# Optimization experiments

Measured on AMD Instinct MI355X. Metric: run time of the kernel, lower is better.

Reference implementation:

```python
import jax, jax.numpy as jnp
import numpy as np

EPS = 1e-5
C = 1.0
SQRT_C = 1.0
MAX_NORM = 0.95


def _log0(y):
    # log map at origin: atanh(sqrt(c)||y||) * y / (sqrt(c)||y||)
    norm = jnp.clip(jnp.linalg.norm(y, axis=-1, keepdims=True), EPS)
    arg = jnp.clip(SQRT_C * norm, None, 1.0 - EPS)
    return jnp.arctanh(arg) * y / (SQRT_C * norm)


def _exp0(v):
    # exp map at origin: tanh(sqrt(c)||v||) * v / (sqrt(c)||v||)
    norm = jnp.clip(jnp.linalg.norm(v, axis=-1, keepdims=True), EPS)
    return jnp.tanh(SQRT_C * norm) * v / (SQRT_C * norm)


def _proj(x):
    # project onto Poincare ball of radius MAX_NORM/sqrt(c)
    max_r = MAX_NORM / SQRT_C
    norm = jnp.linalg.norm(x, axis=-1, keepdims=True)
    return jnp.where(norm > max_r, x * max_r / jnp.clip(norm, EPS), x)


def _hyp_linear(x, W, b):
    # log -> euclidean linear -> exp -> project
    v = _log0(x)
    v = v @ W.T + b
    return _proj(_exp0(v))


def _hyp_graph_conv(x, src, dst, n_nodes, Wm, bm, Wu, bu):
    # 1. hyperbolic linear message transform
    h = _hyp_linear(x, Wm, bm)
    # 2. tangent-space (hyperbolic) mean aggregation over incoming edges
    t = _log0(h[src])                                   # [E, D]
    summed = jax.ops.segment_sum(t, dst, num_segments=n_nodes)
    cnt = jax.ops.segment_sum(jnp.ones((src.shape[0], 1), t.dtype), dst,
                              num_segments=n_nodes)
    agg = _proj(_exp0(summed / jnp.clip(cnt, 1.0)))
    # 3. hyperbolic linear update
    return _hyp_linear(agg, Wu, bu)


def setup_inputs() -> dict:
    key = jax.random.key(0)
    k1, k2, k3, k4 = jax.random.split(key, 4)
    N, E, D, L = 50000, 800000, 128, 2
    x = jax.random.normal(k1, (N, D), dtype=jnp.float32) * 0.01
    edge_index = jax.random.randint(k2, (2, E), 0, N, dtype=jnp.int32)
    msg_W = jax.random.normal(k3, (L, D, D), dtype=jnp.float32) * 0.05
    msg_b = jnp.zeros((L, D), dtype=jnp.float32)
    upd_W = jax.random.normal(k4, (L, D, D), dtype=jnp.float32) * 0.05
    upd_b = jnp.zeros((L, D), dtype=jnp.float32)
    return {"x": x, "edge_index": edge_index, "msg_W": msg_W, "msg_b": msg_b,
            "upd_W": upd_W, "upd_b": upd_b}


def reference(x, edge_index, msg_W, msg_b, upd_W, upd_b):
    src, dst = edge_index[0], edge_index[1]
    n_nodes = x.shape[0]
    h = x
    for l in range(msg_W.shape[0]):  # small fixed layer count
        h = _hyp_graph_conv(h, src, dst, n_nodes,
                            msg_W[l], msg_b[l], upd_W[l], upd_b[l])
    return h
```

## Files before the change

### kernel.cpp

```cpp
#include <hip/hip_runtime.h>
#include <math.h>

#define EPSF 1e-5f
#define MAXN 0.95f
#define DD 128

typedef unsigned short u16;
typedef __attribute__((ext_vector_type(8))) __bf16 bf16x8;
typedef __attribute__((ext_vector_type(4))) float f32x4;
typedef __attribute__((ext_vector_type(8))) unsigned short u16x8;
typedef __attribute__((ext_vector_type(4))) unsigned u32x4;

__device__ __forceinline__ u16 f2bf(float f) {
    unsigned u = __float_as_uint(f);
    return (u16)((u + 0x7FFFu + ((u >> 16) & 1u)) >> 16);
}
__device__ __forceinline__ float bf2f(u16 b) {
    return __uint_as_float(((unsigned)b) << 16);
}

__device__ __forceinline__ float chain_scale(float nrm, bool log_out) {
    float nc  = fmaxf(nrm, EPSF);
    float f   = tanhf(nc) / nc;
    float wn  = f * nrm;
    float p   = (wn > MAXN) ? (MAXN / fmaxf(wn, EPSF)) : 1.f;
    float s   = f * p;
    if (log_out) {
        float n2  = wn * p;
        float n2c = fmaxf(n2, EPSF);
        float arg = fminf(n2c, 1.f - EPSF);
        s *= atanhf(arg) / n2c;
    }
    return s;
}

__global__ __launch_bounds__(256)
void split_w(const float* __restrict__ msgW, const float* __restrict__ updW,
             u16* __restrict__ whi, u16* __restrict__ wlo, int L)
{
    int gid = blockIdx.x * 256 + threadIdx.x;
    int total = L * 2 * DD * DD;
    if (gid >= total) return;
    int mat = gid >> 14;
    int elem = gid & (DD * DD - 1);
    int l = mat >> 1, tpe = mat & 1;
    float f = (tpe ? updW : msgW)[(size_t)l * DD * DD + elem];
    u16 hb = f2bf(f);
    whi[gid] = hb;
    wlo[gid] = f2bf(f - bf2f(hb));
}

template<int LOG_OUT, int LO_OUT, int FP32_OUT, int F32_IN, int SCALE_IN>
__global__ __launch_bounds__(256)
void mfma_linear(const u16* __restrict__ vhi, const u16* __restrict__ vlo,
                 const float* __restrict__ xin, const float* __restrict__ sIn,
                 const u16* __restrict__ whi, const u16* __restrict__ wlo,
                 const float* __restrict__ bias,
                 u16* __restrict__ ohi, u16* __restrict__ olo,
                 float* __restrict__ ofp, int N)
{
    __shared__ float sred[4][64];
    __shared__ float sScale[64];
    __shared__ float sSin[SCALE_IN ? 64 : 1];
    __shared__ u16 sHi[FP32_OUT ? 1 : 64][144];
    __shared__ u16 sLo[LO_OUT ? 64 : 1][144];

    const int tid  = threadIdx.x;
    const int w    = tid >> 6;
    const int lane = tid & 63;
    const int l15  = lane & 15, lk = lane >> 4;
    const int base = blockIdx.x * 64;

    if (SCALE_IN) {
        if (tid < 64) {
            int rg = base + tid;
            sSin[tid] = sIn[rg < N ? rg : (N - 1)];
        }
        __syncthreads();
    }

    bf16x8 wh[2][4], wl[2][4];
    #pragma unroll
    for (int nt = 0; nt < 2; ++nt) {
        const int j = w * 32 + nt * 16 + l15;
        #pragma unroll
        for (int kt = 0; kt < 4; ++kt) {
            const int off = j * DD + kt * 32 + lk * 8;
            wh[nt][kt] = *(const bf16x8*)(whi + off);
            wl[nt][kt] = *(const bf16x8*)(wlo + off);
        }
    }
    const float bv0 = bias[w * 32 + l15];
    const float bv1 = bias[w * 32 + 16 + l15];

    f32x4 acc[4][2];
    #pragma unroll
    for (int mt = 0; mt < 4; ++mt)
        #pragma unroll
        for (int nt = 0; nt < 2; ++nt)
            acc[mt][nt] = (f32x4){0.f, 0.f, 0.f, 0.f};

    #pragma unroll
    for (int mt = 0; mt < 4; ++mt) {
        int row = base + mt * 16 + l15;
        row = (row < N) ? row : (N - 1);
        bf16x8 ah[4], al[4];
        if (F32_IN) {
            const float* xr = xin + (size_t)row * DD + lk * 8;
            float fv[32];
            float ss = 0.f;
            #pragma unroll
            for (int kt = 0; kt < 4; ++kt) {
                float4 a = *(const float4*)(xr + kt * 32);
                float4 b = *(const float4*)(xr + kt * 32 + 4);
                fv[kt*8+0]=a.x; fv[kt*8+1]=a.y; fv[kt*8+2]=a.z; fv[kt*8+3]=a.w;
                fv[kt*8+4]=b.x; fv[kt*8+5]=b.y; fv[kt*8+6]=b.z; fv[kt*8+7]=b.w;
            }
            #pragma unroll
            for (int q = 0; q < 32; ++q) ss += fv[q] * fv[q];
            ss += __shfl_xor(ss, 16);
            ss += __shfl_xor(ss, 32);
            float nc = fmaxf(sqrtf(ss), EPSF);
            float sc = atanhf(fminf(nc, 1.f - EPSF)) / nc;
            #pragma unroll
            for (int kt = 0; kt < 4; ++kt) {
                u16x8 uh, ul;
                #pragma unroll
                for (int q = 0; q < 8; ++q) {
                    float t = fv[kt*8+q] * sc;
                    u16 hb = f2bf(t);
                    uh[q] = hb;
                    ul[q] = f2bf(t - bf2f(hb));
                }
                ah[kt] = *reinterpret_cast<bf16x8*>(&uh);
                al[kt] = *reinterpret_cast<bf16x8*>(&ul);
            }
        } else {
            const size_t ro = (size_t)row * DD + lk * 8;
            #pragma unroll
            for (int kt = 0; kt < 4; ++kt) {
                ah[kt] = *(const bf16x8*)(vhi + ro + kt * 32);
                al[kt] = *(const bf16x8*)(vlo + ro + kt * 32);
            }
        }
        #pragma unroll
        for (int kt = 0; kt < 4; ++kt) {
            #pragma unroll
            for (int nt = 0; nt < 2; ++nt) {
                acc[mt][nt] = __builtin_amdgcn_mfma_f32_16x16x32_bf16(
                    ah[kt], wh[nt][kt], acc[mt][nt], 0, 0, 0);
                acc[mt][nt] = __builtin_amdgcn_mfma_f32_16x16x32_bf16(
                    al[kt], wh[nt][kt], acc[mt][nt], 0, 0, 0);
                acc[mt][nt] = __builtin_amdgcn_mfma_f32_16x16x32_bf16(
                    ah[kt], wl[nt][kt], acc[mt][nt], 0, 0, 0);
            }
        }
    }

    #pragma unroll
    for (int mt = 0; mt < 4; ++mt) {
        #pragma unroll
        for (int r = 0; r < 4; ++r) {
            const float sv = SCALE_IN ? sSin[mt*16 + lk*4 + r] : 1.f;
            float y0 = acc[mt][0][r] * sv + bv0;
            float y1 = acc[mt][1][r] * sv + bv1;
            float part = y0 * y0 + y1 * y1;
            part += __shfl_xor(part, 1);
            part += __shfl_xor(part, 2);
            part += __shfl_xor(part, 4);
            part += __shfl_xor(part, 8);
            if (l15 == 0) sred[w][mt*16 + lk*4 + r] = part;
        }
    }
    __syncthreads();
    if (tid < 64) {
        float ss = sred[0][tid] + sred[1][tid] + sred[2][tid] + sred[3][tid];
        sScale[tid] = chain_scale(sqrtf(ss), LOG_OUT != 0);
    }
    __syncthreads();

    #pragma unroll
    for (int mt = 0; mt < 4; ++mt) {
        #pragma unroll
        for (int r = 0; r < 4; ++r) {
            const int rloc = mt*16 + lk*4 + r;
            const float s = sScale[rloc];
            const float sv = SCALE_IN ? sSin[rloc] : 1.f;
            #pragma unroll
            for (int nt = 0; nt < 2; ++nt) {
                float z = (acc[mt][nt][r] * sv + (nt ? bv1 : bv0)) * s;
                const int col = w*32 + nt*16 + l15;
                if (FP32_OUT) {
                    const int rg = base + rloc;
                    if (rg < N) ofp[(size_t)rg * DD + col] = z;
                } else {
                    u16 hb = f2bf(z);
                    sHi[rloc][col] = hb;
                    if (LO_OUT) sLo[rloc][col] = f2bf(z - bf2f(hb));
                }
            }
        }
    }
    if (!FP32_OUT) {
        __syncthreads();
        const int row = tid >> 2, qc = (tid & 3) * 32;
        const int rg = base + row;
        if (rg < N) {
            #pragma unroll
            for (int i = 0; i < 4; ++i)
                *(u16x8*)(ohi + (size_t)rg * DD + qc + i*8) =
                    *(const u16x8*)(&sHi[row][qc + i*8]);
            if (LO_OUT) {
                #pragma unroll
                for (int i = 0; i < 4; ++i)
                    *(u16x8*)(olo + (size_t)rg * DD + qc + i*8) =
                        *(const u16x8*)(&sLo[row][qc + i*8]);
            }
        }
    }
}

__global__ __launch_bounds__(256)
void degree_rank(const int* __restrict__ dst, int* __restrict__ deg,
                 int* __restrict__ rank, int E)
{
    int e4 = (blockIdx.x * 256 + threadIdx.x) * 4;
    if (e4 + 3 < E) {
        int4 d = *(const int4*)(dst + e4);
        int4 r;
        r.x = atomicAdd(&deg[d.x], 1);
        r.y = atomicAdd(&deg[d.y], 1);
        r.z = atomicAdd(&deg[d.z], 1);
        r.w = atomicAdd(&deg[d.w], 1);
        *(int4*)(rank + e4) = r;
    } else {
        for (int e = e4; e < E; ++e) rank[e] = atomicAdd(&deg[dst[e]], 1);
    }
}

__global__ __launch_bounds__(1024)
void scan_rowptr(const int* __restrict__ deg, int* __restrict__ rowptr, int N)
{
    __shared__ int wsum[16];
    const int t = threadIdx.x, wv = t >> 6, ln = t & 63;
    int carry = 0;
    const int nch = (N + 4095) / 4096;
    for (int c = 0; c < nch; ++c) {
        const int i = c * 4096 + t * 4;
        int4 d = *(const int4*)(deg + i);
        int e1 = d.x, e2 = e1 + d.y, e3 = e2 + d.z, tot = e3 + d.w;
        int sc = tot;
        #pragma unroll
        for (int off = 1; off < 64; off <<= 1) {
            int u = __shfl_up(sc, off);
            if (ln >= off) sc += u;
        }
        if (ln == 63) wsum[wv] = sc;
        __syncthreads();
        if (wv == 0 && ln < 16) {
            int s2 = wsum[ln];
            #pragma unroll
            for (int off = 1; off < 16; off <<= 1) {
                int u = __shfl_up(s2, off);
                if (ln >= off) s2 += u;
            }
            wsum[ln] = s2;
        }
        __syncthreads();
        const int off0 = carry + ((wv > 0) ? wsum[wv - 1] : 0) + (sc - tot);
        if (i + 3 < N) {
            *(int4*)(rowptr + i) = make_int4(off0, off0 + e1, off0 + e2, off0 + e3);
        } else {
            if (i     < N) rowptr[i]     = off0;
            if (i + 1 < N) rowptr[i + 1] = off0 + e1;
            if (i + 2 < N) rowptr[i + 2] = off0 + e2;
        }
        carry += wsum[15];
        __syncthreads();
    }
    if (t == 0) rowptr[N] = carry;
}

__global__ __launch_bounds__(256)
void fill_csr(const int* __restrict__ src, const int* __restrict__ dst,
              const int* __restrict__ rowptr, const int* __restrict__ rank,
              int* __restrict__ csr, int E)
{
    int e4 = (blockIdx.x * 256 + threadIdx.x) * 4;
    if (e4 + 3 < E) {
        int4 d = *(const int4*)(dst + e4);
        int4 r = *(const int4*)(rank + e4);
        int4 s = *(const int4*)(src + e4);
        csr[rowptr[d.x] + r.x] = s.x;
        csr[rowptr[d.y] + r.y] = s.y;
        csr[rowptr[d.z] + r.z] = s.z;
        csr[rowptr[d.w] + r.w] = s.w;
    } else {
        for (int e = e4; e < E; ++e) csr[rowptr[dst[e]] + rank[e]] = src[e];
    }
}

__global__ __launch_bounds__(256)
void csr_gather_sum(const u16* __restrict__ ghi, const int* __restrict__ rowptr,
                    const int* __restrict__ csr, u16* __restrict__ ohi,
                    u16* __restrict__ olo, float* __restrict__ ssum, int N)
{
    int node = blockIdx.x * 4 + (threadIdx.x >> 6);
    if (node >= N) return;
    const int lane = threadIdx.x & 63;
    const int eg = lane >> 4, l15 = lane & 15;
    const int beg = rowptr[node], end = rowptr[node + 1];

    float acc[8] = {0.f,0.f,0.f,0.f,0.f,0.f,0.f,0.f};
    for (int b = beg; b < end; b += 64) {
        const int cnt = min(end - b, 64);
        const int myidx = (lane < cnt) ? csr[b + lane] : 0;
        u32x4 vc;
        {
            const bool act = eg < cnt;
            const int s = __shfl(myidx, act ? eg : 0);
            if (act) vc = *(const u32x4*)(ghi + (size_t)s * DD + l15 * 8);
        }
        for (int j = 0; j < cnt; j += 4) {
            const int en = j + 4 + eg;
            const bool actn = en < cnt;
            const int sn = __shfl(myidx, actn ? en : 0);
            u32x4 vn;
            if (actn) vn = *(const u32x4*)(ghi + (size_t)sn * DD + l15 * 8);
            if (j + eg < cnt) {
                #pragma unroll
                for (int p = 0; p < 4; ++p) {
                    acc[2*p+0] += __uint_as_float(vc[p] << 16);
                    acc[2*p+1] += __uint_as_float(vc[p] & 0xffff0000u);
                }
            }
            vc = vn;
        }
    }
    #pragma unroll
    for (int q = 0; q < 8; ++q) {
        acc[q] += __shfl_xor(acc[q], 16);
        acc[q] += __shfl_xor(acc[q], 32);
    }
    float ss = 0.f;
    #pragma unroll
    for (int q = 0; q < 8; ++q) ss += acc[q] * acc[q];
    ss += __shfl_xor(ss, 1); ss += __shfl_xor(ss, 2);
    ss += __shfl_xor(ss, 4); ss += __shfl_xor(ss, 8);
    if (eg == 0) {
        u32x4 hw, lw;
        #pragma unroll
        for (int p = 0; p < 4; ++p) {
            u16 h0 = f2bf(acc[2*p+0]), h1 = f2bf(acc[2*p+1]);
            hw[p] = (unsigned)h0 | ((unsigned)h1 << 16);
            u16 l0 = f2bf(acc[2*p+0] - bf2f(h0));
            u16 l1 = f2bf(acc[2*p+1] - bf2f(h1));
            lw[p] = (unsigned)l0 | ((unsigned)l1 << 16);
        }
        *(u32x4*)(ohi + (size_t)node * DD + l15 * 8) = hw;
        *(u32x4*)(olo + (size_t)node * DD + l15 * 8) = lw;
        if (l15 == 0) ssum[node] = ss;
    }
}

__global__ __launch_bounds__(256)
void node_scale(const float* __restrict__ ssum, const int* __restrict__ rowptr,
                float* __restrict__ sout, int N)
{
    int n = blockIdx.x * 256 + threadIdx.x;
    if (n >= N) return;
    int cnt = max(rowptr[n + 1] - rowptr[n], 1);
    float inv = 1.f / (float)cnt;
    float nrm = sqrtf(ssum[n]) * inv;
    sout[n] = chain_scale(nrm, true) * inv;
}

extern "C" void kernel_launch(void* const* d_in, const int* in_sizes, int n_in,
                              void* d_out, int out_size, void* d_ws, size_t ws_size,
                              hipStream_t stream)
{
    const float* x     = (const float*)d_in[0];
    const int*   ei    = (const int*)d_in[1];
    const float* msg_W = (const float*)d_in[2];
    const float* msg_b = (const float*)d_in[3];
    const float* upd_W = (const float*)d_in[4];
    const float* upd_b = (const float*)d_in[5];

    const int N = in_sizes[0] / DD;
    const int E = in_sizes[1] / 2;
    const int L = in_sizes[2] / (DD * DD);

    const int* src = ei;
    const int* dst = ei + E;

    u16* Ahi  = (u16*)d_ws;
    u16* Alo  = Ahi + (size_t)N * DD;
    u16* WhiA = Alo + (size_t)N * DD;
    u16* WloA = WhiA + (size_t)2 * L * DD * DD;
    int* deg  = (int*)(WloA + (size_t)2 * L * DD * DD);
    const int degCap = ((N + 4095) / 4096) * 4096;
    int* rowptr = deg + degCap;
    int* csr    = rowptr + (N + 1);
    float* ssum   = (float*)(csr + E);
    float* sscale = ssum + N;

    u16* Bhi = (u16*)d_out;
    u16* Blo = Bhi + (size_t)N * DD;
    int* rank = (int*)Blo;

    u16* bufHi[2] = {Ahi, Bhi};
    u16* bufLo[2] = {Alo, Blo};
    int cur = (L % 2 == 0) ? 1 : 0;

    const int nodeBlocks = (N + 63) / 64;
    const int aggBlocks  = (N + 3) / 4;
    const int edge4Blocks = ((E + 3) / 4 + 255) / 256;

    hipMemsetAsync(deg, 0, (size_t)degCap * sizeof(int), stream);
    degree_rank<<<edge4Blocks, 256, 0, stream>>>(dst, deg, rank, E);
    scan_rowptr<<<1, 1024, 0, stream>>>(deg, rowptr, N);
    fill_csr<<<edge4Blocks, 256, 0, stream>>>(src, dst, rowptr, rank, csr, E);
    split_w<<<(2 * L * DD * DD + 255) / 256, 256, 0, stream>>>(
        msg_W, upd_W, WhiA, WloA, L);

    for (int l = 0; l < L; ++l) {
        const u16* wmh = WhiA + (size_t)(l * 2 + 0) * DD * DD;
        const u16* wml = WloA + (size_t)(l * 2 + 0) * DD * DD;
        const u16* wuh = WhiA + (size_t)(l * 2 + 1) * DD * DD;
        const u16* wul = WloA + (size_t)(l * 2 + 1) * DD * DD;

        if (l == 0)
            mfma_linear<1, 0, 0, 1, 0><<<nodeBlocks, 256, 0, stream>>>(
                nullptr, nullptr, x, nullptr, wmh, wml, msg_b + (size_t)l * DD,
                bufHi[cur ^ 1], nullptr, nullptr, N);
        else
            mfma_linear<1, 0, 0, 0, 0><<<nodeBlocks, 256, 0, stream>>>(
                bufHi[cur], bufLo[cur], nullptr, nullptr, wmh, wml,
                msg_b + (size_t)l * DD, bufHi[cur ^ 1], nullptr, nullptr, N);
        cur ^= 1;

        csr_gather_sum<<<aggBlocks, 256, 0, stream>>>(
            bufHi[cur], rowptr, csr, bufHi[cur ^ 1], bufLo[cur ^ 1], ssum, N);
        cur ^= 1;

        node_scale<<<(N + 255) / 256, 256, 0, stream>>>(ssum, rowptr, sscale, N);

        if (l == L - 1)
            mfma_linear<0, 0, 1, 0, 1><<<nodeBlocks, 256, 0, stream>>>(
                bufHi[cur], bufLo[cur], nullptr, sscale, wuh, wul,
                upd_b + (size_t)l * DD, nullptr, nullptr, (float*)d_out, N);
        else
            mfma_linear<1, 1, 0, 0, 1><<<nodeBlocks, 256, 0, stream>>>(
                bufHi[cur], bufLo[cur], nullptr, sscale, wuh, wul,
                upd_b + (size_t)l * DD, bufHi[cur ^ 1], bufLo[cur ^ 1], nullptr, N);
        cur ^= 1;
    }
}
```

Baseline: 277.5 us.

## Fuse update and next message linear, inline node scale, drop lo outputs

Merges the update linear of layer l with the message linear of layer l+1 into one kernel. The intermediate hi/lo bf16 activations stay in LDS instead of making a global round trip. The separate node_scale kernel is removed and its per-row scale is computed inline from ssum and rowptr. The memset is replaced by a small zeroing kernel, and the LDS row padding changes. This cuts launches and global traffic, but the fused kernel uses more LDS and registers, which may lower occupancy.

```diff
diff --git a/kernel.cpp b/kernel.cpp
--- a/kernel.cpp
+++ b/kernel.cpp
@@ -34,6 +34,21 @@
     return s;
 }
 
+__device__ __forceinline__ float agg_scale(const float* __restrict__ ssum,
+                                           const int* __restrict__ rowptr,
+                                           int rg) {
+    int cnt = max(rowptr[rg + 1] - rowptr[rg], 1);
+    float inv = 1.f / (float)cnt;
+    return chain_scale(sqrtf(ssum[rg]) * inv, true) * inv;
+}
+
+__global__ __launch_bounds__(256)
+void zero_int4(int4* __restrict__ p, int n4)
+{
+    int i = blockIdx.x * 256 + threadIdx.x;
+    if (i < n4) p[i] = make_int4(0, 0, 0, 0);
+}
+
 __global__ __launch_bounds__(256)
 void split_w(const float* __restrict__ msgW, const float* __restrict__ updW,
              u16* __restrict__ whi, u16* __restrict__ wlo, int L)
@@ -50,20 +65,19 @@
     wlo[gid] = f2bf(f - bf2f(hb));
 }
 
-template<int LOG_OUT, int LO_OUT, int FP32_OUT, int F32_IN, int SCALE_IN>
+template<int LOG_OUT, int FP32_OUT, int F32_IN, int SCALE_IN>
 __global__ __launch_bounds__(256)
 void mfma_linear(const u16* __restrict__ vhi, const u16* __restrict__ vlo,
-                 const float* __restrict__ xin, const float* __restrict__ sIn,
+                 const float* __restrict__ xin,
+                 const float* __restrict__ ssum, const int* __restrict__ rowptr,
                  const u16* __restrict__ whi, const u16* __restrict__ wlo,
                  const float* __restrict__ bias,
-                 u16* __restrict__ ohi, u16* __restrict__ olo,
-                 float* __restrict__ ofp, int N)
+                 u16* __restrict__ ohi, float* __restrict__ ofp, int N)
 {
     __shared__ float sred[4][64];
     __shared__ float sScale[64];
     __shared__ float sSin[SCALE_IN ? 64 : 1];
-    __shared__ u16 sHi[FP32_OUT ? 1 : 64][144];
-    __shared__ u16 sLo[LO_OUT ? 64 : 1][144];
+    __shared__ u16 sHi[FP32_OUT ? 1 : 64][136];
 
     const int tid  = threadIdx.x;
     const int w    = tid >> 6;
@@ -74,7 +88,7 @@
     if (SCALE_IN) {
         if (tid < 64) {
             int rg = base + tid;
-            sSin[tid] = sIn[rg < N ? rg : (N - 1)];
+            sSin[tid] = agg_scale(ssum, rowptr, rg < N ? rg : (N - 1));
         }
         __syncthreads();
     }
@@ -194,9 +208,7 @@
                     const int rg = base + rloc;
                     if (rg < N) ofp[(size_t)rg * DD + col] = z;
                 } else {
-                    u16 hb = f2bf(z);
-                    sHi[rloc][col] = hb;
-                    if (LO_OUT) sLo[rloc][col] = f2bf(z - bf2f(hb));
+                    sHi[rloc][col] = f2bf(z);
                 }
             }
         }
@@ -210,12 +222,211 @@
             for (int i = 0; i < 4; ++i)
                 *(u16x8*)(ohi + (size_t)rg * DD + qc + i*8) =
                     *(const u16x8*)(&sHi[row][qc + i*8]);
-            if (LO_OUT) {
+        }
+    }
+}
+
+__global__ __launch_bounds__(256)
+void mfma_linear_fused(const u16* __restrict__ vhi, const u16* __restrict__ vlo,
+                       const float* __restrict__ ssum, const int* __restrict__ rowptr,
+                       const u16* __restrict__ wuh, const u16* __restrict__ wul,
+                       const float* __restrict__ bu,
+                       const u16* __restrict__ wmh, const u16* __restrict__ wml,
+                       const float* __restrict__ bm,
+                       u16* __restrict__ ohi, int N)
+{
+    __shared__ float sred[4][64];
+    __shared__ float sScale[64];
+    __shared__ float sSin[64];
+    __shared__ u16 sHi[64][136];
+    __shared__ u16 sLo[64][136];
+
+    const int tid  = threadIdx.x;
+    const int w    = tid >> 6;
+    const int lane = tid & 63;
+    const int l15  = lane & 15, lk = lane >> 4;
+    const int base = blockIdx.x * 64;
+
+    if (tid < 64) {
+        int rg = base + tid;
+        sSin[tid] = agg_scale(ssum, rowptr, rg < N ? rg : (N - 1));
+    }
+    __syncthreads();
+
+    f32x4 acc[4][2];
+
+    {
+        bf16x8 wh[2][4], wl[2][4];
+        #pragma unroll
+        for (int nt = 0; nt < 2; ++nt) {
+            const int j = w * 32 + nt * 16 + l15;
+            #pragma unroll
+            for (int kt = 0; kt < 4; ++kt) {
+                const int off = j * DD + kt * 32 + lk * 8;
+                wh[nt][kt] = *(const bf16x8*)(wuh + off);
+                wl[nt][kt] = *(const bf16x8*)(wul + off);
+            }
+        }
+        const float bv0 = bu[w * 32 + l15];
+        const float bv1 = bu[w * 32 + 16 + l15];
+
+        #pragma unroll
+        for (int mt = 0; mt < 4; ++mt)
+            #pragma unroll
+            for (int nt = 0; nt < 2; ++nt)
+                acc[mt][nt] = (f32x4){0.f, 0.f, 0.f, 0.f};
+
+        #pragma unroll
+        for (int mt = 0; mt < 4; ++mt) {
+            int row = base + mt * 16 + l15;
+            row = (row < N) ? row : (N - 1);
+            const size_t ro = (size_t)row * DD + lk * 8;
+            bf16x8 ah[4], al[4];
+            #pragma unroll
+            for (int kt = 0; kt < 4; ++kt) {
+                ah[kt] = *(const bf16x8*)(vhi + ro + kt * 32);
+                al[kt] = *(const bf16x8*)(vlo + ro + kt * 32);
+            }
+            #pragma unroll
+            for (int kt = 0; kt < 4; ++kt) {
                 #pragma unroll
-                for (int i = 0; i < 4; ++i)
-                    *(u16x8*)(olo + (size_t)rg * DD + qc + i*8) =
-                        *(const u16x8*)(&sLo[row][qc + i*8]);
-            }
+                for (int nt = 0; nt < 2; ++nt) {
+                    acc[mt][nt] = __builtin_amdgcn_mfma_f32_16x16x32_bf16(
+                        ah[kt], wh[nt][kt], acc[mt][nt], 0, 0, 0);
+                    acc[mt][nt] = __builtin_amdgcn_mfma_f32_16x16x32_bf16(
+                        al[kt], wh[nt][kt], acc[mt][nt], 0, 0, 0);
+                    acc[mt][nt] = __builtin_amdgcn_mfma_f32_16x16x32_bf16(
+                        ah[kt], wl[nt][kt], acc[mt][nt], 0, 0, 0);
+                }
+            }
+        }
+
+        #pragma unroll
+        for (int mt = 0; mt < 4; ++mt) {
+            #pragma unroll
+            for (int r = 0; r < 4; ++r) {
+                const float sv = sSin[mt*16 + lk*4 + r];
+                float y0 = acc[mt][0][r] * sv + bv0;
+                float y1 = acc[mt][1][r] * sv + bv1;
+                float part = y0 * y0 + y1 * y1;
+                part += __shfl_xor(part, 1);
+                part += __shfl_xor(part, 2);
+                part += __shfl_xor(part, 4);
+                part += __shfl_xor(part, 8);
+                if (l15 == 0) sred[w][mt*16 + lk*4 + r] = part;
+            }
+        }
+        __syncthreads();
+        if (tid < 64) {
+            float ss = sred[0][tid] + sred[1][tid] + sred[2][tid] + sred[3][tid];
+            sScale[tid] = chain_scale(sqrtf(ss), true);
+        }
+        __syncthreads();
+        #pragma unroll
+        for (int mt = 0; mt < 4; ++mt) {
+            #pragma unroll
+            for (int r = 0; r < 4; ++r) {
+                const int rloc = mt*16 + lk*4 + r;
+                const float s = sScale[rloc];
+                const float sv = sSin[rloc];
+                #pragma unroll
+                for (int nt = 0; nt < 2; ++nt) {
+                    float z = (acc[mt][nt][r] * sv + (nt ? bv1 : bv0)) * s;
+                    const int col = w*32 + nt*16 + l15;
+                    u16 hb = f2bf(z);
+                    sHi[rloc][col] = hb;
+                    sLo[rloc][col] = f2bf(z - bf2f(hb));
+                }
+            }
+        }
+    }
+    __syncthreads();
+
+    {
+        bf16x8 wh[2][4], wl[2][4];
+        #pragma unroll
+        for (int nt = 0; nt < 2; ++nt) {
+            const int j = w * 32 + nt * 16 + l15;
+            #pragma unroll
+            for (int kt = 0; kt < 4; ++kt) {
+                const int off = j * DD + kt * 32 + lk * 8;
+                wh[nt][kt] = *(const bf16x8*)(wmh + off);
+                wl[nt][kt] = *(const bf16x8*)(wml + off);
+            }
+        }
+        const float bv0 = bm[w * 32 + l15];
+        const float bv1 = bm[w * 32 + 16 + l15];
+
+        #pragma unroll
+        for (int mt = 0; mt < 4; ++mt)
+            #pragma unroll
+            for (int nt = 0; nt < 2; ++nt)
+                acc[mt][nt] = (f32x4){0.f, 0.f, 0.f, 0.f};
+
+        #pragma unroll
+        for (int mt = 0; mt < 4; ++mt) {
+            const int r16 = mt * 16 + l15;
+            bf16x8 ah[4], al[4];
+            #pragma unroll
+            for (int kt = 0; kt < 4; ++kt) {
+                ah[kt] = *(const bf16x8*)(&sHi[r16][kt * 32 + lk * 8]);
+                al[kt] = *(const bf16x8*)(&sLo[r16][kt * 32 + lk * 8]);
+            }
+            #pragma unroll
+            for (int kt = 0; kt < 4; ++kt) {
+                #pragma unroll
+                for (int nt = 0; nt < 2; ++nt) {
+                    acc[mt][nt] = __builtin_amdgcn_mfma_f32_16x16x32_bf16(
+                        ah[kt], wh[nt][kt], acc[mt][nt], 0, 0, 0);
+                    acc[mt][nt] = __builtin_amdgcn_mfma_f32_16x16x32_bf16(
+                        al[kt], wh[nt][kt], acc[mt][nt], 0, 0, 0);
+                    acc[mt][nt] = __builtin_amdgcn_mfma_f32_16x16x32_bf16(
+                        ah[kt], wl[nt][kt], acc[mt][nt], 0, 0, 0);
+                }
+            }
+        }
+
+        #pragma unroll
+        for (int mt = 0; mt < 4; ++mt) {
+            #pragma unroll
+            for (int r = 0; r < 4; ++r) {
+                float y0 = acc[mt][0][r] + bv0;
+                float y1 = acc[mt][1][r] + bv1;
+                float part = y0 * y0 + y1 * y1;
+                part += __shfl_xor(part, 1);
+                part += __shfl_xor(part, 2);
+                part += __shfl_xor(part, 4);
+                part += __shfl_xor(part, 8);
+                if (l15 == 0) sred[w][mt*16 + lk*4 + r] = part;
+            }
+        }
+        __syncthreads();
+        if (tid < 64) {
+            float ss = sred[0][tid] + sred[1][tid] + sred[2][tid] + sred[3][tid];
+            sScale[tid] = chain_scale(sqrtf(ss), true);
+        }
+        __syncthreads();
+        #pragma unroll
+        for (int mt = 0; mt < 4; ++mt) {
+            #pragma unroll
+            for (int r = 0; r < 4; ++r) {
+                const int rloc = mt*16 + lk*4 + r;
+                const float s = sScale[rloc];
+                #pragma unroll
+                for (int nt = 0; nt < 2; ++nt) {
+                    float z = (acc[mt][nt][r] + (nt ? bv1 : bv0)) * s;
+                    sHi[rloc][w*32 + nt*16 + l15] = f2bf(z);
+                }
+            }
+        }
+        __syncthreads();
+        const int row = tid >> 2, qc = (tid & 3) * 32;
+        const int rg = base + row;
+        if (rg < N) {
+            #pragma unroll
+            for (int i = 0; i < 4; ++i)
+                *(u16x8*)(ohi + (size_t)rg * DD + qc + i*8) =
+                    *(const u16x8*)(&sHi[row][qc + i*8]);
         }
     }
 }
@@ -363,18 +574,6 @@
     }
 }
 
-__global__ __launch_bounds__(256)
-void node_scale(const float* __restrict__ ssum, const int* __restrict__ rowptr,
-                float* __restrict__ sout, int N)
-{
-    int n = blockIdx.x * 256 + threadIdx.x;
-    if (n >= N) return;
-    int cnt = max(rowptr[n + 1] - rowptr[n], 1);
-    float inv = 1.f / (float)cnt;
-    float nrm = sqrtf(ssum[n]) * inv;
-    sout[n] = chain_scale(nrm, true) * inv;
-}
-
 extern "C" void kernel_launch(void* const* d_in, const int* in_sizes, int n_in,
                               void* d_out, int out_size, void* d_ws, size_t ws_size,
                               hipStream_t stream)
@@ -401,58 +600,47 @@
     const int degCap = ((N + 4095) / 4096) * 4096;
     int* rowptr = deg + degCap;
     int* csr    = rowptr + (N + 1);
-    float* ssum   = (float*)(csr + E);
-    float* sscale = ssum + N;
-
-    u16* Bhi = (u16*)d_out;
-    u16* Blo = Bhi + (size_t)N * DD;
+    float* ssum = (float*)(csr + E);
+
+    u16* Bhi  = (u16*)d_out;
+    u16* Blo  = Bhi + (size_t)N * DD;
     int* rank = (int*)Blo;
 
-    u16* bufHi[2] = {Ahi, Bhi};
-    u16* bufLo[2] = {Alo, Blo};
-    int cur = (L % 2 == 0) ? 1 : 0;
-
-    const int nodeBlocks = (N + 63) / 64;
-    const int aggBlocks  = (N + 3) / 4;
+    const int nodeBlocks  = (N + 63) / 64;
+    const int aggBlocks   = (N + 3) / 4;
     const int edge4Blocks = ((E + 3) / 4 + 255) / 256;
 
-    hipMemsetAsync(deg, 0, (size_t)degCap * sizeof(int), stream);
+    zero_int4<<<(degCap / 4 + 255) / 256, 256, 0, stream>>>((int4*)deg, degCap / 4);
     degree_rank<<<edge4Blocks, 256, 0, stream>>>(dst, deg, rank, E);
     scan_rowptr<<<1, 1024, 0, stream>>>(deg, rowptr, N);
     fill_csr<<<edge4Blocks, 256, 0, stream>>>(src, dst, rowptr, rank, csr, E);
     split_w<<<(2 * L * DD * DD + 255) / 256, 256, 0, stream>>>(
         msg_W, upd_W, WhiA, WloA, L);
 
+    mfma_linear<1, 0, 1, 0><<<nodeBlocks, 256, 0, stream>>>(
+        nullptr, nullptr, x, nullptr, nullptr,
+        WhiA, WloA, msg_b, Bhi, nullptr, N);
+
     for (int l = 0; l < L; ++l) {
-        const u16* wmh = WhiA + (size_t)(l * 2 + 0) * DD * DD;
-        const u16* wml = WloA + (size_t)(l * 2 + 0) * DD * DD;
         const u16* wuh = WhiA + (size_t)(l * 2 + 1) * DD * DD;
         const u16* wul = WloA + (size_t)(l * 2 + 1) * DD * DD;
 
-        if (l == 0)
-            mfma_linear<1, 0, 0, 1, 0><<<nodeBlocks, 256, 0, stream>>>(
-                nullptr, nullptr, x, nullptr, wmh, wml, msg_b + (size_t)l * DD,
-                bufHi[cur ^ 1], nullptr, nullptr, N);
-        else
-            mfma_linear<1, 0, 0, 0, 0><<<nodeBlocks, 256, 0, stream>>>(
-                bufHi[cur], bufLo[cur], nullptr, nullptr, wmh, wml,
-                msg_b + (size_t)l * DD, bufHi[cur ^ 1], nullptr, nullptr, N);
-        cur ^= 1;
-
         csr_gather_sum<<<aggBlocks, 256, 0, stream>>>(
-            bufHi[cur], rowptr, csr, bufHi[cur ^ 1], bufLo[cur ^ 1], ssum, N);
-        cur ^= 1;
-
-        node_scale<<<(N + 255) / 256, 256, 0, stream>>>(ssum, rowptr, sscale, N);
-
-        if (l == L - 1)
-            mfma_linear<0, 0, 1, 0, 1><<<nodeBlocks, 256, 0, stream>>>(
-                bufHi[cur], bufLo[cur], nullptr, sscale, wuh, wul,
-                upd_b + (size_t)l * DD, nullptr, nullptr, (float*)d_out, N);
-        else
-            mfma_linear<1, 1, 0, 0, 1><<<nodeBlocks, 256, 0, stream>>>(
-                bufHi[cur], bufLo[cur], nullptr, sscale, wuh, wul,
-                upd_b + (size_t)l * DD, bufHi[cur ^ 1], bufLo[cur ^ 1], nullptr, N);
-        cur ^= 1;
-    }
-}
+            Bhi, rowptr, csr, Ahi, Alo, ssum, N);
+
+        if (l < L - 1) {
+            const u16* wmh = WhiA + (size_t)((l + 1) * 2 + 0) * DD * DD;
+            const u16* wml = WloA + (size_t)((l + 1) * 2 + 0) * DD * DD;
+            mfma_linear_fused<<<nodeBlocks, 256, 0, stream>>>(
+                Ahi, Alo, ssum, rowptr,
+                wuh, wul, upd_b + (size_t)l * DD,
+                wmh, wml, msg_b + (size_t)(l + 1) * DD,
+                Bhi, N);
+        } else {
+            mfma_linear<0, 1, 0, 1><<<nodeBlocks, 256, 0, stream>>>(
+                Ahi, Alo, nullptr, ssum, rowptr,
+                wuh, wul, upd_b + (size_t)l * DD,
+                nullptr, (float*)d_out, N);
+        }
+    }
+}
```

After: 255.1 us. -8.1%, faster.

## Fuse update and next message linear, fold node scale into GEMM, per-wave row tiles

Applied to the files above, without the earlier changes.

The MFMA linear kernel is restructured so each wave owns 16 rows and all 128 output columns. The row-norm reduction becomes an in-wave shuffle instead of cross-wave shared-memory reductions with block barriers. The node_scale kernel is removed: the per-node aggregation scale is computed inline from ssum and rowptr. The update linear of layer l and the message linear of layer l+1 are fused into one kernel that passes the intermediate through swizzled LDS, which also drops the lo-part global write. Weights are now streamed from global or cache per MFMA rather than held in registers, and the memset is replaced by a small zeroing kernel.

```diff
diff --git a/kernel.cpp b/kernel.cpp
--- a/kernel.cpp
+++ b/kernel.cpp
@@ -10,6 +10,8 @@
 typedef __attribute__((ext_vector_type(4))) float f32x4;
 typedef __attribute__((ext_vector_type(8))) unsigned short u16x8;
 typedef __attribute__((ext_vector_type(4))) unsigned u32x4;
+
+#define MFMA16 __builtin_amdgcn_mfma_f32_16x16x32_bf16
 
 __device__ __forceinline__ u16 f2bf(float f) {
     unsigned u = __float_as_uint(f);
@@ -34,6 +36,284 @@
     return s;
 }
 
+__device__ __forceinline__ float agg_scale(const float* __restrict__ ssum,
+                                           const int* __restrict__ rowptr,
+                                           int rg) {
+    int cnt = max(rowptr[rg + 1] - rowptr[rg], 1);
+    float inv = 1.f / (float)cnt;
+    return chain_scale(sqrtf(ssum[rg]) * inv, true) * inv;
+}
+
+__device__ __forceinline__ void gemm16(const bf16x8 ah[4], const bf16x8 al[4],
+                                       const u16* __restrict__ whi,
+                                       const u16* __restrict__ wlo,
+                                       int l15, int lk, f32x4 acc[8])
+{
+    #pragma unroll
+    for (int kt = 0; kt < 4; ++kt) {
+        #pragma unroll
+        for (int nt = 0; nt < 8; ++nt) {
+            const int off = (nt * 16 + l15) * DD + kt * 32 + lk * 8;
+            const bf16x8 wwh = *(const bf16x8*)(whi + off);
+            const bf16x8 wwl = *(const bf16x8*)(wlo + off);
+            acc[nt] = MFMA16(ah[kt], wwh, acc[nt], 0, 0, 0);
+            acc[nt] = MFMA16(al[kt], wwh, acc[nt], 0, 0, 0);
+            acc[nt] = MFMA16(ah[kt], wwl, acc[nt], 0, 0, 0);
+        }
+    }
+}
+
+__device__ __forceinline__ void loadA_bf(const u16* __restrict__ vhi,
+                                         const u16* __restrict__ vlo,
+                                         size_t ro, bf16x8 ah[4], bf16x8 al[4])
+{
+    #pragma unroll
+    for (int kt = 0; kt < 4; ++kt) {
+        ah[kt] = *(const bf16x8*)(vhi + ro + kt * 32);
+        al[kt] = *(const bf16x8*)(vlo + ro + kt * 32);
+    }
+}
+
+__device__ __forceinline__ void loadA_f32log(const float* __restrict__ xr,
+                                             bf16x8 ah[4], bf16x8 al[4])
+{
+    float fv[32]; float ss = 0.f;
+    #pragma unroll
+    for (int kt = 0; kt < 4; ++kt) {
+        float4 a = *(const float4*)(xr + kt * 32);
+        float4 b = *(const float4*)(xr + kt * 32 + 4);
+        fv[kt*8+0]=a.x; fv[kt*8+1]=a.y; fv[kt*8+2]=a.z; fv[kt*8+3]=a.w;
+        fv[kt*8+4]=b.x; fv[kt*8+5]=b.y; fv[kt*8+6]=b.z; fv[kt*8+7]=b.w;
+    }
+    #pragma unroll
+    for (int q = 0; q < 32; ++q) ss += fv[q] * fv[q];
+    ss += __shfl_xor(ss, 16);
+    ss += __shfl_xor(ss, 32);
+    float nc = fmaxf(sqrtf(ss), EPSF);
+    float sc = atanhf(fminf(nc, 1.f - EPSF)) / nc;
+    #pragma unroll
+    for (int kt = 0; kt < 4; ++kt) {
+        u16x8 uh, ul;
+        #pragma unroll
+        for (int q = 0; q < 8; ++q) {
+            float t = fv[kt*8+q] * sc;
+            u16 hb = f2bf(t);
+            uh[q] = hb;
+            ul[q] = f2bf(t - bf2f(hb));
+        }
+        ah[kt] = *reinterpret_cast<bf16x8*>(&uh);
+        al[kt] = *reinterpret_cast<bf16x8*>(&ul);
+    }
+}
+
+__device__ __forceinline__ void store_g_staged(u16* __restrict__ sg,
+                                               const f32x4 acc[8],
+                                               const float bv[8],
+                                               const float svr[4],
+                                               const float sr[4],
+                                               int l15, int lk, int lane,
+                                               int rowbase, u16* __restrict__ ohi,
+                                               int N)
+{
+    #pragma unroll
+    for (int r = 0; r < 4; ++r) {
+        const int row = lk * 4 + r;
+        const int key = (row & 7) << 3;
+        #pragma unroll
+        for (int nt = 0; nt < 8; ++nt) {
+            const int col = nt * 16 + l15;
+            float z = fmaf(acc[nt][r], svr[r], bv[nt]) * sr[r];
+            sg[row * 128 + ((col & ~7) ^ key) + (col & 7)] = f2bf(z);
+        }
+    }
+    asm volatile("s_waitcnt lgkmcnt(0)" ::: "memory");
+    __builtin_amdgcn_sched_barrier(0);
+    {
+        const int row = lane >> 2;
+        const int rg = rowbase + row;
+        const int key = (row & 7) << 3;
+        if (rg < N) {
+            #pragma unroll
+            for (int i = 0; i < 4; ++i) {
+                const int lc = (lane & 3) * 4 + i;
+                u16x8 v = *(const u16x8*)(sg + row * 128 + ((lc << 3) ^ key));
+                *(u16x8*)(ohi + (size_t)rg * DD + lc * 8) = v;
+            }
+        }
+    }
+}
+
+template<int LOG_OUT, int FP32_OUT, int F32_IN, int SCALE_IN>
+__global__ __launch_bounds__(256, 3)
+void mfma_linear(const u16* __restrict__ vhi, const u16* __restrict__ vlo,
+                 const float* __restrict__ xin,
+                 const float* __restrict__ ssum, const int* __restrict__ rowptr,
+                 const u16* __restrict__ whi, const u16* __restrict__ wlo,
+                 const float* __restrict__ bias,
+                 u16* __restrict__ ohi, float* __restrict__ ofp, int N)
+{
+    __shared__ u16 sStage[FP32_OUT ? 4 : 4 * 16 * 128];
+
+    const int tid  = threadIdx.x;
+    const int w    = tid >> 6;
+    const int lane = tid & 63;
+    const int l15  = lane & 15, lk = lane >> 4;
+    const int rowbase = blockIdx.x * 64 + w * 16;
+
+    const int arow = min(rowbase + l15, N - 1);
+    float sv_l = 1.f;
+    if (SCALE_IN) sv_l = agg_scale(ssum, rowptr, arow);
+
+    bf16x8 ah[4], al[4];
+    if (F32_IN) loadA_f32log(xin + (size_t)arow * DD + lk * 8, ah, al);
+    else        loadA_bf(vhi, vlo, (size_t)arow * DD + lk * 8, ah, al);
+
+    f32x4 acc[8];
+    #pragma unroll
+    for (int nt = 0; nt < 8; ++nt) acc[nt] = (f32x4){0.f, 0.f, 0.f, 0.f};
+    gemm16(ah, al, whi, wlo, l15, lk, acc);
+
+    float bv[8];
+    #pragma unroll
+    for (int nt = 0; nt < 8; ++nt) bv[nt] = bias[nt * 16 + l15];
+
+    float sr[4], svr[4];
+    #pragma unroll
+    for (int r = 0; r < 4; ++r) {
+        svr[r] = SCALE_IN ? __shfl(sv_l, lk * 4 + r) : 1.f;
+        float part = 0.f;
+        #pragma unroll
+        for (int nt = 0; nt < 8; ++nt) {
+            float y = fmaf(acc[nt][r], svr[r], bv[nt]);
+            part += y * y;
+        }
+        part += __shfl_xor(part, 1); part += __shfl_xor(part, 2);
+        part += __shfl_xor(part, 4); part += __shfl_xor(part, 8);
+        sr[r] = chain_scale(sqrtf(part), LOG_OUT != 0);
+    }
+
+    if (FP32_OUT) {
+        #pragma unroll
+        for (int r = 0; r < 4; ++r) {
+            const int rg = rowbase + lk * 4 + r;
+            if (rg < N) {
+                #pragma unroll
+                for (int nt = 0; nt < 8; ++nt)
+                    ofp[(size_t)rg * DD + nt * 16 + l15] =
+                        fmaf(acc[nt][r], svr[r], bv[nt]) * sr[r];
+            }
+        }
+    } else {
+        store_g_staged(sStage + w * (16 * 128), acc, bv, svr, sr,
+                       l15, lk, lane, rowbase, ohi, N);
+    }
+}
+
+__global__ __launch_bounds__(256, 3)
+void mfma_linear_fused(const u16* __restrict__ vhi, const u16* __restrict__ vlo,
+                       const float* __restrict__ ssum, const int* __restrict__ rowptr,
+                       const u16* __restrict__ wuh, const u16* __restrict__ wul,
+                       const float* __restrict__ bu,
+                       const u16* __restrict__ wmh, const u16* __restrict__ wml,
+                       const float* __restrict__ bm,
+                       u16* __restrict__ ohi, int N)
+{
+    __shared__ float sT[4][16 * 128];
+
+    const int tid  = threadIdx.x;
+    const int w    = tid >> 6;
+    const int lane = tid & 63;
+    const int l15  = lane & 15, lk = lane >> 4;
+    const int rowbase = blockIdx.x * 64 + w * 16;
+    float* st = sT[w];
+
+    const int arow = min(rowbase + l15, N - 1);
+    float sv_l = agg_scale(ssum, rowptr, arow);
+
+    bf16x8 ah[4], al[4];
+    loadA_bf(vhi, vlo, (size_t)arow * DD + lk * 8, ah, al);
+
+    f32x4 acc[8];
+    #pragma unroll
+    for (int nt = 0; nt < 8; ++nt) acc[nt] = (f32x4){0.f, 0.f, 0.f, 0.f};
+    gemm16(ah, al, wuh, wul, l15, lk, acc);
+
+    float bv[8];
+    #pragma unroll
+    for (int nt = 0; nt < 8; ++nt) bv[nt] = bu[nt * 16 + l15];
+
+    #pragma unroll
+    for (int r = 0; r < 4; ++r) {
+        const float sv = __shfl(sv_l, lk * 4 + r);
+        float part = 0.f;
+        #pragma unroll
+        for (int nt = 0; nt < 8; ++nt) {
+            float y = fmaf(acc[nt][r], sv, bv[nt]);
+            part += y * y;
+        }
+        part += __shfl_xor(part, 1); part += __shfl_xor(part, 2);
+        part += __shfl_xor(part, 4); part += __shfl_xor(part, 8);
+        const float s = chain_scale(sqrtf(part), true);
+        const int row = lk * 4 + r;
+        const int key = row & 7;
+        #pragma unroll
+        for (int nt = 0; nt < 8; ++nt) {
+            const int col = nt * 16 + l15;
+            float z = fmaf(acc[nt][r], sv, bv[nt]) * s;
+            st[row * 128 + (((col >> 2) ^ key) << 2) + (col & 3)] = z;
+        }
+    }
+    asm volatile("s_waitcnt lgkmcnt(0)" ::: "memory");
+    __builtin_amdgcn_sched_barrier(0);
+
+    #pragma unroll
+    for (int kt = 0; kt < 4; ++kt) {
+        const int key = l15 & 7;
+        const int c0 = kt * 8 + lk * 2;
+        float4 f0 = *(const float4*)(st + l15 * 128 + (((c0    ) ^ key) << 2));
+        float4 f1 = *(const float4*)(st + l15 * 128 + (((c0 + 1) ^ key) << 2));
+        float f[8] = {f0.x, f0.y, f0.z, f0.w, f1.x, f1.y, f1.z, f1.w};
+        u16x8 uh, ul;
+        #pragma unroll
+        for (int q = 0; q < 8; ++q) {
+            u16 hb = f2bf(f[q]);
+            uh[q] = hb;
+            ul[q] = f2bf(f[q] - bf2f(hb));
+        }
+        ah[kt] = *reinterpret_cast<bf16x8*>(&uh);
+        al[kt] = *reinterpret_cast<bf16x8*>(&ul);
+    }
+    #pragma unroll
+    for (int nt = 0; nt < 8; ++nt) acc[nt] = (f32x4){0.f, 0.f, 0.f, 0.f};
+    gemm16(ah, al, wmh, wml, l15, lk, acc);
+
+    #pragma unroll
+    for (int nt = 0; nt < 8; ++nt) bv[nt] = bm[nt * 16 + l15];
+
+    float sr[4], svr[4];
+    #pragma unroll
+    for (int r = 0; r < 4; ++r) {
+        svr[r] = 1.f;
+        float part = 0.f;
+        #pragma unroll
+        for (int nt = 0; nt < 8; ++nt) {
+            float y = acc[nt][r] + bv[nt];
+            part += y * y;
+        }
+        part += __shfl_xor(part, 1); part += __shfl_xor(part, 2);
+        part += __shfl_xor(part, 4); part += __shfl_xor(part, 8);
+        sr[r] = chain_scale(sqrtf(part), true);
+    }
+    store_g_staged((u16*)st, acc, bv, svr, sr, l15, lk, lane, rowbase, ohi, N);
+}
+
+__global__ __launch_bounds__(256)
+void zero_int4(int4* __restrict__ p, int n4)
+{
+    int i = blockIdx.x * 256 + threadIdx.x;
+    if (i < n4) p[i] = make_int4(0, 0, 0, 0);
+}
+
 __global__ __launch_bounds__(256)
 void split_w(const float* __restrict__ msgW, const float* __restrict__ updW,
              u16* __restrict__ whi, u16* __restrict__ wlo, int L)
@@ -48,176 +328,6 @@
     u16 hb = f2bf(f);
     whi[gid] = hb;
     wlo[gid] = f2bf(f - bf2f(hb));
-}
-
-template<int LOG_OUT, int LO_OUT, int FP32_OUT, int F32_IN, int SCALE_IN>
-__global__ __launch_bounds__(256)
-void mfma_linear(const u16* __restrict__ vhi, const u16* __restrict__ vlo,
-                 const float* __restrict__ xin, const float* __restrict__ sIn,
-                 const u16* __restrict__ whi, const u16* __restrict__ wlo,
-                 const float* __restrict__ bias,
-                 u16* __restrict__ ohi, u16* __restrict__ olo,
-                 float* __restrict__ ofp, int N)
-{
-    __shared__ float sred[4][64];
-    __shared__ float sScale[64];
-    __shared__ float sSin[SCALE_IN ? 64 : 1];
-    __shared__ u16 sHi[FP32_OUT ? 1 : 64][144];
-    __shared__ u16 sLo[LO_OUT ? 64 : 1][144];
-
-    const int tid  = threadIdx.x;
-    const int w    = tid >> 6;
-    const int lane = tid & 63;
-    const int l15  = lane & 15, lk = lane >> 4;
-    const int base = blockIdx.x * 64;
-
-    if (SCALE_IN) {
-        if (tid < 64) {
-            int rg = base + tid;
-            sSin[tid] = sIn[rg < N ? rg : (N - 1)];
-        }
-        __syncthreads();
-    }
-
-    bf16x8 wh[2][4], wl[2][4];
-    #pragma unroll
-    for (int nt = 0; nt < 2; ++nt) {
-        const int j = w * 32 + nt * 16 + l15;
-        #pragma unroll
-        for (int kt = 0; kt < 4; ++kt) {
-            const int off = j * DD + kt * 32 + lk * 8;
-            wh[nt][kt] = *(const bf16x8*)(whi + off);
-            wl[nt][kt] = *(const bf16x8*)(wlo + off);
-        }
-    }
-    const float bv0 = bias[w * 32 + l15];
-    const float bv1 = bias[w * 32 + 16 + l15];
-
-    f32x4 acc[4][2];
-    #pragma unroll
-    for (int mt = 0; mt < 4; ++mt)
-        #pragma unroll
-        for (int nt = 0; nt < 2; ++nt)
-            acc[mt][nt] = (f32x4){0.f, 0.f, 0.f, 0.f};
-
-    #pragma unroll
-    for (int mt = 0; mt < 4; ++mt) {
-        int row = base + mt * 16 + l15;
-        row = (row < N) ? row : (N - 1);
-        bf16x8 ah[4], al[4];
-        if (F32_IN) {
-            const float* xr = xin + (size_t)row * DD + lk * 8;
-            float fv[32];
-            float ss = 0.f;
-            #pragma unroll
-            for (int kt = 0; kt < 4; ++kt) {
-                float4 a = *(const float4*)(xr + kt * 32);
-                float4 b = *(const float4*)(xr + kt * 32 + 4);
-                fv[kt*8+0]=a.x; fv[kt*8+1]=a.y; fv[kt*8+2]=a.z; fv[kt*8+3]=a.w;
-                fv[kt*8+4]=b.x; fv[kt*8+5]=b.y; fv[kt*8+6]=b.z; fv[kt*8+7]=b.w;
-            }
-            #pragma unroll
-            for (int q = 0; q < 32; ++q) ss += fv[q] * fv[q];
-            ss += __shfl_xor(ss, 16);
-            ss += __shfl_xor(ss, 32);
-            float nc = fmaxf(sqrtf(ss), EPSF);
-            float sc = atanhf(fminf(nc, 1.f - EPSF)) / nc;
-            #pragma unroll
-            for (int kt = 0; kt < 4; ++kt) {
-                u16x8 uh, ul;
-                #pragma unroll
-                for (int q = 0; q < 8; ++q) {
-                    float t = fv[kt*8+q] * sc;
-                    u16 hb = f2bf(t);
-                    uh[q] = hb;
-                    ul[q] = f2bf(t - bf2f(hb));
-                }
-                ah[kt] = *reinterpret_cast<bf16x8*>(&uh);
-                al[kt] = *reinterpret_cast<bf16x8*>(&ul);
-            }
-        } else {
-            const size_t ro = (size_t)row * DD + lk * 8;
-            #pragma unroll
-            for (int kt = 0; kt < 4; ++kt) {
-                ah[kt] = *(const bf16x8*)(vhi + ro + kt * 32);
-                al[kt] = *(const bf16x8*)(vlo + ro + kt * 32);
-            }
-        }
-        #pragma unroll
-        for (int kt = 0; kt < 4; ++kt) {
-            #pragma unroll
-            for (int nt = 0; nt < 2; ++nt) {
-                acc[mt][nt] = __builtin_amdgcn_mfma_f32_16x16x32_bf16(
-                    ah[kt], wh[nt][kt], acc[mt][nt], 0, 0, 0);
-                acc[mt][nt] = __builtin_amdgcn_mfma_f32_16x16x32_bf16(
-                    al[kt], wh[nt][kt], acc[mt][nt], 0, 0, 0);
-                acc[mt][nt] = __builtin_amdgcn_mfma_f32_16x16x32_bf16(
-                    ah[kt], wl[nt][kt], acc[mt][nt], 0, 0, 0);
-            }
-        }
-    }
-
-    #pragma unroll
-    for (int mt = 0; mt < 4; ++mt) {
-        #pragma unroll
-        for (int r = 0; r < 4; ++r) {
-            const float sv = SCALE_IN ? sSin[mt*16 + lk*4 + r] : 1.f;
-            float y0 = acc[mt][0][r] * sv + bv0;
-            float y1 = acc[mt][1][r] * sv + bv1;
-            float part = y0 * y0 + y1 * y1;
-            part += __shfl_xor(part, 1);
-            part += __shfl_xor(part, 2);
-            part += __shfl_xor(part, 4);
-            part += __shfl_xor(part, 8);
-            if (l15 == 0) sred[w][mt*16 + lk*4 + r] = part;
-        }
-    }
-    __syncthreads();
-    if (tid < 64) {
-        float ss = sred[0][tid] + sred[1][tid] + sred[2][tid] + sred[3][tid];
-        sScale[tid] = chain_scale(sqrtf(ss), LOG_OUT != 0);
-    }
-    __syncthreads();
-
-    #pragma unroll
-    for (int mt = 0; mt < 4; ++mt) {
-        #pragma unroll
-        for (int r = 0; r < 4; ++r) {
-            const int rloc = mt*16 + lk*4 + r;
-            const float s = sScale[rloc];
-            const float sv = SCALE_IN ? sSin[rloc] : 1.f;
-            #pragma unroll
-            for (int nt = 0; nt < 2; ++nt) {
-                float z = (acc[mt][nt][r] * sv + (nt ? bv1 : bv0)) * s;
-                const int col = w*32 + nt*16 + l15;
-                if (FP32_OUT) {
-                    const int rg = base + rloc;
-                    if (rg < N) ofp[(size_t)rg * DD + col] = z;
-                } else {
-                    u16 hb = f2bf(z);
-                    sHi[rloc][col] = hb;
-                    if (LO_OUT) sLo[rloc][col] = f2bf(z - bf2f(hb));
-                }
-            }
-        }
-    }
-    if (!FP32_OUT) {
-        __syncthreads();
-        const int row = tid >> 2, qc = (tid & 3) * 32;
-        const int rg = base + row;
-        if (rg < N) {
-            #pragma unroll
-            for (int i = 0; i < 4; ++i)
-                *(u16x8*)(ohi + (size_t)rg * DD + qc + i*8) =
-                    *(const u16x8*)(&sHi[row][qc + i*8]);
-            if (LO_OUT) {
-                #pragma unroll
-                for (int i = 0; i < 4; ++i)
-                    *(u16x8*)(olo + (size_t)rg * DD + qc + i*8) =
-                        *(const u16x8*)(&sLo[row][qc + i*8]);
-            }
-        }
-    }
 }
 
 __global__ __launch_bounds__(256)
@@ -363,18 +473,6 @@
     }
 }
 
-__global__ __launch_bounds__(256)
-void node_scale(const float* __restrict__ ssum, const int* __restrict__ rowptr,
-                float* __restrict__ sout, int N)
-{
-    int n = blockIdx.x * 256 + threadIdx.x;
-    if (n >= N) return;
-    int cnt = max(rowptr[n + 1] - rowptr[n], 1);
-    float inv = 1.f / (float)cnt;
-    float nrm = sqrtf(ssum[n]) * inv;
-    sout[n] = chain_scale(nrm, true) * inv;
-}
-
 extern "C" void kernel_launch(void* const* d_in, const int* in_sizes, int n_in,
                               void* d_out, int out_size, void* d_ws, size_t ws_size,
                               hipStream_t stream)
@@ -401,58 +499,47 @@
     const int degCap = ((N + 4095) / 4096) * 4096;
     int* rowptr = deg + degCap;
     int* csr    = rowptr + (N + 1);
-    float* ssum   = (float*)(csr + E);
-    float* sscale = ssum + N;
-
-    u16* Bhi = (u16*)d_out;
-    u16* Blo = Bhi + (size_t)N * DD;
+    float* ssum = (float*)(csr + E);
+
+    u16* Bhi  = (u16*)d_out;
+    u16* Blo  = Bhi + (size_t)N * DD;
     int* rank = (int*)Blo;
 
-    u16* bufHi[2] = {Ahi, Bhi};
-    u16* bufLo[2] = {Alo, Blo};
-    int cur = (L % 2 == 0) ? 1 : 0;
-
-    const int nodeBlocks = (N + 63) / 64;
-    const int aggBlocks  = (N + 3) / 4;
+    const int nodeBlocks  = (N + 63) / 64;
+    const int aggBlocks   = (N + 3) / 4;
     const int edge4Blocks = ((E + 3) / 4 + 255) / 256;
 
-    hipMemsetAsync(deg, 0, (size_t)degCap * sizeof(int), stream);
+    zero_int4<<<(degCap / 4 + 255) / 256, 256, 0, stream>>>((int4*)deg, degCap / 4);
     degree_rank<<<edge4Blocks, 256, 0, stream>>>(dst, deg, rank, E);
     scan_rowptr<<<1, 1024, 0, stream>>>(deg, rowptr, N);
     fill_csr<<<edge4Blocks, 256, 0, stream>>>(src, dst, rowptr, rank, csr, E);
     split_w<<<(2 * L * DD * DD + 255) / 256, 256, 0, stream>>>(
         msg_W, upd_W, WhiA, WloA, L);
 
+    mfma_linear<1, 0, 1, 0><<<nodeBlocks, 256, 0, stream>>>(
+        nullptr, nullptr, x, nullptr, nullptr,
+        WhiA, WloA, msg_b, Bhi, nullptr, N);
+
     for (int l = 0; l < L; ++l) {
-        const u16* wmh = WhiA + (size_t)(l * 2 + 0) * DD * DD;
-        const u16* wml = WloA + (size_t)(l * 2 + 0) * DD * DD;
         const u16* wuh = WhiA + (size_t)(l * 2 + 1) * DD * DD;
         const u16* wul = WloA + (size_t)(l * 2 + 1) * DD * DD;
 
-        if (l == 0)
-            mfma_linear<1, 0, 0, 1, 0><<<nodeBlocks, 256, 0, stream>>>(
-                nullptr, nullptr, x, nullptr, wmh, wml, msg_b + (size_t)l * DD,
-                bufHi[cur ^ 1], nullptr, nullptr, N);
-        else
-            mfma_linear<1, 0, 0, 0, 0><<<nodeBlocks, 256, 0, stream>>>(
-                bufHi[cur], bufLo[cur], nullptr, nullptr, wmh, wml,
-                msg_b + (size_t)l * DD, bufHi[cur ^ 1], nullptr, nullptr, N);
-        cur ^= 1;
-
         csr_gather_sum<<<aggBlocks, 256, 0, stream>>>(
-            bufHi[cur], rowptr, csr, bufHi[cur ^ 1], bufLo[cur ^ 1], ssum, N);
-        cur ^= 1;
-
-        node_scale<<<(N + 255) / 256, 256, 0, stream>>>(ssum, rowptr, sscale, N);
-
-        if (l == L - 1)
-            mfma_linear<0, 0, 1, 0, 1><<<nodeBlocks, 256, 0, stream>>>(
-                bufHi[cur], bufLo[cur], nullptr, sscale, wuh, wul,
-                upd_b + (size_t)l * DD, nullptr, nullptr, (float*)d_out, N);
-        else
-            mfma_linear<1, 1, 0, 0, 1><<<nodeBlocks, 256, 0, stream>>>(
-                bufHi[cur], bufLo[cur], nullptr, sscale, wuh, wul,
-                upd_b + (size_t)l * DD, bufHi[cur ^ 1], bufLo[cur ^ 1], nullptr, N);
-        cur ^= 1;
-    }
-}
+            Bhi, rowptr, csr, Ahi, Alo, ssum, N);
+
+        if (l < L - 1) {
+            const u16* wmh = WhiA + (size_t)((l + 1) * 2 + 0) * DD * DD;
+            const u16* wml = WloA + (size_t)((l + 1) * 2 + 0) * DD * DD;
+            mfma_linear_fused<<<nodeBlocks, 256, 0, stream>>>(
+                Ahi, Alo, ssum, rowptr,
+                wuh, wul, upd_b + (size_t)l * DD,
+                wmh, wml, msg_b + (size_t)(l + 1) * DD,
+                Bhi, N);
+        } else {
+            mfma_linear<0, 1, 0, 1><<<nodeBlocks, 256, 0, stream>>>(
+                Ahi, Alo, nullptr, ssum, rowptr,
+                wuh, wul, upd_b + (size_t)l * DD,
+                nullptr, (float*)d_out, N);
+        }
+    }
+}
```

Result: slower. 301.0 us (+8.4%).
